# Kernel optimization log

Measured on AMD Instinct MI355X. Metric: run time of the kernel, lower is better.

The kernel has to match this reference:

```python
import jax, jax.numpy as jnp
import numpy as np

K = 8
W_CONST = 0.01
EPS = 1e-8


def _normalize(v, eps=1e-8):
    return v / (jnp.linalg.norm(v, axis=-1, keepdims=True) + eps)


def _coarse_normal(x, vertices, vertex_normals):
    # x: (N,3); vertices, vertex_normals: (V,3)
    # brute-force KNN (ascending by squared distance, like cKDTree.query)
    d2_all = jnp.sum((x[:, None, :] - vertices[None, :, :]) ** 2, axis=-1)  # (N,V)
    neg_d2, idx = jax.lax.top_k(-d2_all, K)  # sorted ascending distance
    d2 = -neg_d2                                                    # (N,K)
    v_knn = vertices[idx]                                           # (N,K,3)
    n_knn = vertex_normals[idx]                                     # (N,K,3)
    d2c = jnp.maximum(d2, EPS)
    inv_d2 = 1.0 / d2c                                              # (N,K)
    term_knn = jnp.sum(n_knn * inv_d2[..., None], axis=1)           # (N,3)
    v1 = v_knn[:, 0]                                                # nearest vertex
    d2_v1 = jnp.maximum(jnp.sum((x - v1) ** 2, axis=-1), EPS)       # (N,)
    term_dir = (x - v1) / (W_CONST * d2_v1[:, None])
    W = jnp.sum(inv_d2, axis=1) + 1.0 / W_CONST                     # (N,)
    n_tilde = (term_knn + term_dir) / W[:, None]
    nc = _normalize(n_tilde)
    return nc, v1


def _ray_mesh_first_hit(origins, dirs, tri0, e1, e2):
    # Moller-Trumbore, all points vs all faces. origins/dirs: (N,3); tri0/e1/e2: (F,3)
    pvec = jnp.cross(dirs[:, None, :], e2[None, :, :])              # (N,F,3)
    det = jnp.einsum('fk,nfk->nf', e1, pvec)                        # (N,F)
    ok_det = jnp.abs(det) > EPS
    inv_det = jnp.where(ok_det, 1.0 / jnp.where(ok_det, det, 1.0), 0.0)
    tvec = origins[:, None, :] - tri0[None, :, :]                   # (N,F,3)
    u = jnp.sum(tvec * pvec, axis=-1) * inv_det
    qvec = jnp.cross(tvec, e1[None, :, :])                          # (N,F,3)
    v = jnp.einsum('nk,nfk->nf', dirs, qvec) * inv_det
    t = jnp.einsum('fk,nfk->nf', e2, qvec) * inv_det
    valid = ok_det & (u >= 0.0) & (v >= 0.0) & (u + v <= 1.0) & (t > EPS)
    t_masked = jnp.where(valid, t, jnp.inf)
    t_min = jnp.min(t_masked, axis=1)                               # first hit along ray
    hit = jnp.isfinite(t_min)
    loc = origins + dirs * jnp.where(hit, t_min, 0.0)[:, None]
    return hit, loc


def _project(x, vertices, vertex_normals, faces):
    nc, v1 = _coarse_normal(x, vertices, vertex_normals)
    tri0 = vertices[faces[:, 0]]
    e1 = vertices[faces[:, 1]] - tri0
    e2 = vertices[faces[:, 2]] - tri0
    # primary cast along -nc
    hit1, loc1 = _ray_mesh_first_hit(x, -nc, tri0, e1, e2)
    # fallback cast toward nearest vertex
    dir_fb = _normalize(v1 - x)
    hit2, loc2 = _ray_mesh_first_hit(x, dir_fb, tri0, e1, e2)
    xc = jnp.where(hit1[:, None], loc1, jnp.where(hit2[:, None], loc2, v1))
    s = jnp.sum((x - xc) * nc, axis=-1, keepdims=True)              # (N,1)
    return xc, s, nc


def setup_inputs() -> dict:
    key = jax.random.key(0)
    k1, k2, k3, k4 = jax.random.split(key, 4)
    N, V, F = 2048, 8192, 8192
    x = jax.random.normal(k1, (N, 3), dtype=jnp.float32)
    vertices = jax.random.normal(k2, (V, 3), dtype=jnp.float32)
    vertex_normals = _normalize(jax.random.normal(k3, (V, 3), dtype=jnp.float32))
    faces = jax.random.randint(k4, (F, 3), 0, V, dtype=jnp.int32)
    return {"x": x, "vertices": vertices, "vertex_normals": vertex_normals, "faces": faces}


def reference(x, vertices, vertex_normals, faces):
    # returns (xc:(N,3), s:(N,1), nc:(N,3)) like ProjectionFn.forward
    return _project(x, vertices, vertex_normals, faces)
```

## Files before the change

kernel.cpp:

```cpp
#include <hip/hip_runtime.h>
#include <math.h>

#pragma float_control(precise, on)

#define EPSF 1e-8f


__global__ void __launch_bounds__(256) knn_prep_kernel(
    const float* __restrict__ x, const float* __restrict__ verts,
    const float* __restrict__ vnorm, const int* __restrict__ faces,
    float* __restrict__ tri, float* __restrict__ ncw,
    float* __restrict__ v1w, float* __restrict__ dfbw,
    int N, int V, int F) {
#pragma clang fp contract(off)
    int p = blockIdx.x;
    int tid = threadIdx.x;
    int wave = tid >> 6;
    int lane = tid & 63;
    if (p >= N) return;

    int gt = p * 256 + tid;
    if (gt < F) {
        int f0 = faces[gt * 3 + 0];
        int f1 = faces[gt * 3 + 1];
        int f2 = faces[gt * 3 + 2];
        float t0x = verts[f0 * 3 + 0], t0y = verts[f0 * 3 + 1], t0z = verts[f0 * 3 + 2];
        float ax = verts[f1 * 3 + 0], ay = verts[f1 * 3 + 1], az = verts[f1 * 3 + 2];
        float bx = verts[f2 * 3 + 0], by = verts[f2 * 3 + 1], bz = verts[f2 * 3 + 2];
        float4* t4 = (float4*)(tri + gt * 12);
        t4[0] = make_float4(t0x, t0y, t0z, ax - t0x);
        t4[1] = make_float4(ay - t0y, az - t0z, bx - t0x, by - t0y);
        t4[2] = make_float4(bz - t0z, 0.f, 0.f, 0.f);
    }

    float xx = x[p * 3 + 0];
    float xy = x[p * 3 + 1];
    float xz = x[p * 3 + 2];

    unsigned long long ka[8], kb[8];
#pragma unroll
    for (int i = 0; i < 8; ++i) { ka[i] = ~0ULL; kb[i] = ~0ULL; }

    for (int va = tid; va < V; va += 512) {
        int vb = va + 256;
        bool hasB = vb < V;

        float avx = verts[va * 3 + 0];
        float avy = verts[va * 3 + 1];
        float avz = verts[va * 3 + 2];
        float bvx = 0.f, bvy = 0.f, bvz = 0.f;
        if (hasB) {
            bvx = verts[vb * 3 + 0];
            bvy = verts[vb * 3 + 1];
            bvz = verts[vb * 3 + 2];
        }

        float dxa = xx - avx, dya = xy - avy, dza = xz - avz;
        float d2a = ((dxa * dxa) + (dya * dya)) + (dza * dza);
        unsigned long long kA =
            (((unsigned long long)__float_as_uint(d2a)) << 32) | (unsigned int)va;
        if (kA < ka[7]) {
            ka[7] = kA;
#pragma unroll
            for (int j = 7; j > 0; --j) {
                if (ka[j] < ka[j - 1]) {
                    unsigned long long t = ka[j];
                    ka[j] = ka[j - 1];
                    ka[j - 1] = t;
                }
            }
        }

        if (hasB) {
            float dxb = xx - bvx, dyb = xy - bvy, dzb = xz - bvz;
            float d2b = ((dxb * dxb) + (dyb * dyb)) + (dzb * dzb);
            unsigned long long kB =
                (((unsigned long long)__float_as_uint(d2b)) << 32) | (unsigned int)vb;
            if (kB < kb[7]) {
                kb[7] = kB;
#pragma unroll
                for (int j = 7; j > 0; --j) {
                    if (kb[j] < kb[j - 1]) {
                        unsigned long long t = kb[j];
                        kb[j] = kb[j - 1];
                        kb[j - 1] = t;
                    }
                }
            }
        }
    }

    unsigned long long wsel[8];
#pragma unroll
    for (int j = 0; j < 8; ++j) {
        unsigned long long c = (ka[0] < kb[0]) ? ka[0] : kb[0];
        unsigned long long m = c;
#pragma unroll
        for (int s = 1; s < 64; s <<= 1) {
            unsigned long long o = __shfl_xor(m, s, 64);
            if (o < m) m = o;
        }
        if (c == m) {
            if (ka[0] == m) {
#pragma unroll
                for (int t = 0; t < 7; ++t) ka[t] = ka[t + 1];
                ka[7] = ~0ULL;
            } else {
#pragma unroll
                for (int t = 0; t < 7; ++t) kb[t] = kb[t + 1];
                kb[7] = ~0ULL;
            }
        }
        wsel[j] = m;
    }

    __shared__ unsigned long long cand[32];
    if (lane == 0) {
#pragma unroll
        for (int j = 0; j < 8; ++j) cand[wave * 8 + j] = wsel[j];
    }
    __syncthreads();
    if (wave != 0) return;

    unsigned long long c0 = (lane < 32) ? cand[lane] : ~0ULL;
    unsigned long long sel[8];
#pragma unroll
    for (int j = 0; j < 8; ++j) {
        unsigned long long m = c0;
#pragma unroll
        for (int s = 1; s < 64; s <<= 1) {
            unsigned long long o = __shfl_xor(m, s, 64);
            if (o < m) m = o;
        }
        if (c0 == m) c0 = ~0ULL;
        sel[j] = m;
    }

    if (lane != 0) return;

    float invk[8];
    float nsx = 0.f, nsy = 0.f, nsz = 0.f;
#pragma unroll
    for (int j = 0; j < 8; ++j) {
        int id = (int)(sel[j] & 0xffffffffu);
        float d2 = __uint_as_float((unsigned int)(sel[j] >> 32));
        float inv = 1.0f / fmaxf(d2, EPSF);
        invk[j] = inv;
        nsx = nsx + vnorm[id * 3 + 0] * inv;
        nsy = nsy + vnorm[id * 3 + 1] * inv;
        nsz = nsz + vnorm[id * 3 + 2] * inv;
    }
    float Wsum = ((invk[0] + invk[1]) + (invk[2] + invk[3])) +
                 ((invk[4] + invk[5]) + (invk[6] + invk[7]));

    int id0 = (int)(sel[0] & 0xffffffffu);
    float v1x = verts[id0 * 3 + 0];
    float v1y = verts[id0 * 3 + 1];
    float v1z = verts[id0 * 3 + 2];

    float dxv = xx - v1x, dyv = xy - v1y, dzv = xz - v1z;
    float d2v1 = fmaxf(((dxv * dxv) + (dyv * dyv)) + (dzv * dzv), EPSF);
    float den = 0.01f * d2v1;
    float tdx = dxv / den, tdy = dyv / den, tdz = dzv / den;

    float W = Wsum + 100.0f;
    float ntx = (nsx + tdx) / W;
    float nty = (nsy + tdy) / W;
    float ntz = (nsz + tdz) / W;
    float nrm = sqrtf(((ntx * ntx) + (nty * nty)) + (ntz * ntz)) + 1e-8f;
    float ncx = ntx / nrm, ncy = nty / nrm, ncz = ntz / nrm;

    float fx = v1x - xx, fy = v1y - xy, fz = v1z - xz;
    float fn = sqrtf(((fx * fx) + (fy * fy)) + (fz * fz)) + 1e-8f;
    fx = fx / fn; fy = fy / fn; fz = fz / fn;

    ncw[p * 3 + 0] = ncx; ncw[p * 3 + 1] = ncy; ncw[p * 3 + 2] = ncz;
    v1w[p * 3 + 0] = v1x; v1w[p * 3 + 1] = v1y; v1w[p * 3 + 2] = v1z;
    dfbw[p * 3 + 0] = fx; dfbw[p * 3 + 1] = fy; dfbw[p * 3 + 2] = fz;
}

__global__ void __launch_bounds__(256) ray_fin_kernel(
    const float* __restrict__ x, const float* __restrict__ tri,
    const float* __restrict__ ncw, const float* __restrict__ v1w,
    const float* __restrict__ dfbw, float* __restrict__ out, int N, int F) {
#pragma clang fp contract(off)
    const float M = 1e-5f;
    __shared__ unsigned int red[8];
    int p = blockIdx.x;
    int tid = threadIdx.x;
    int wave = tid >> 6;
    int lane = tid & 63;
    if (p >= N) return;

    float xx = x[p * 3 + 0];
    float xy = x[p * 3 + 1];
    float xz = x[p * 3 + 2];
    float ncx = ncw[p * 3 + 0], ncy = ncw[p * 3 + 1], ncz = ncw[p * 3 + 2];
    float dbx = dfbw[p * 3 + 0], dby = dfbw[p * 3 + 1], dbz = dfbw[p * 3 + 2];
    float dax = -ncx, day = -ncy, daz = -ncz;

    const float INF = __uint_as_float(0x7f800000u);
    float tba = INF, tbb = INF;
    for (int fi = tid; fi < F; fi += 256) {
        const float4 A = *(const float4*)(tri + fi * 12);
        const float4 B = *(const float4*)(tri + fi * 12 + 4);
        const float4 C = *(const float4*)(tri + fi * 12 + 8);
        float e1x = A.w, e1y = B.x, e1z = B.y;
        float e2x = B.z, e2y = B.w, e2z = C.x;

        float tvx = xx - A.x;
        float tvy = xy - A.y;
        float tvz = xz - A.z;
        float qx = (tvy * e1z) - (tvz * e1y);
        float qy = (tvz * e1x) - (tvx * e1z);
        float qz = (tvx * e1y) - (tvy * e1x);
        float tq = ((e2x * qx) + (e2y * qy)) + (e2z * qz);

        {
            float px = (day * e2z) - (daz * e2y);
            float py = (daz * e2x) - (dax * e2z);
            float pz = (dax * e2y) - (day * e2x);
            float det = ((e1x * px) + (e1y * py)) + (e1z * pz);
            bool ok = fabsf(det) > EPSF;
            float inv = ok ? (1.0f / det) : 0.0f;
            float u = (((tvx * px) + (tvy * py)) + (tvz * pz)) * inv;
            float v = (((dax * qx) + (day * qy)) + (daz * qz)) * inv;
            float t = tq * inv;
            bool valid = ok && (u >= -M) && (v >= -M) && ((u + v) <= 1.0f + M) && (t > EPSF);
            tba = (valid && t < tba) ? t : tba;
        }
        {
            float px = (dby * e2z) - (dbz * e2y);
            float py = (dbz * e2x) - (dbx * e2z);
            float pz = (dbx * e2y) - (dby * e2x);
            float det = ((e1x * px) + (e1y * py)) + (e1z * pz);
            bool ok = fabsf(det) > EPSF;
            float inv = ok ? (1.0f / det) : 0.0f;
            float u = (((tvx * px) + (tvy * py)) + (tvz * pz)) * inv;
            float v = (((dbx * qx) + (dby * qy)) + (dbz * qz)) * inv;
            float t = tq * inv;
            bool valid = ok && (u >= -M) && (v >= -M) && ((u + v) <= 1.0f + M) && (t > EPSF);
            tbb = (valid && t < tbb) ? t : tbb;
        }
    }

    unsigned int ma = __float_as_uint(tba);
    unsigned int mb = __float_as_uint(tbb);
#pragma unroll
    for (int s = 1; s < 64; s <<= 1) {
        unsigned int oa = __shfl_xor(ma, s, 64);
        if (oa < ma) ma = oa;
        unsigned int ob = __shfl_xor(mb, s, 64);
        if (ob < mb) mb = ob;
    }
    if (lane == 0) { red[wave * 2 + 0] = ma; red[wave * 2 + 1] = mb; }
    __syncthreads();
    if (tid != 0) return;

    unsigned int u1 = min(min(red[0], red[2]), min(red[4], red[6]));
    unsigned int u2 = min(min(red[1], red[3]), min(red[5], red[7]));
    float t1 = __uint_as_float(u1);
    float t2 = __uint_as_float(u2);
    bool h1 = t1 < INF;
    bool h2 = t2 < INF;

    float xcx, xcy, xcz;
    if (h1) {
        xcx = xx + ((-ncx) * t1);
        xcy = xy + ((-ncy) * t1);
        xcz = xz + ((-ncz) * t1);
    } else if (h2) {
        xcx = xx + (dbx * t2);
        xcy = xy + (dby * t2);
        xcz = xz + (dbz * t2);
    } else {
        xcx = v1w[p * 3 + 0]; xcy = v1w[p * 3 + 1]; xcz = v1w[p * 3 + 2];
    }
    float s = (((xx - xcx) * ncx) + ((xy - xcy) * ncy)) + ((xz - xcz) * ncz);

    out[p * 3 + 0] = xcx;
    out[p * 3 + 1] = xcy;
    out[p * 3 + 2] = xcz;
    out[3 * N + p] = s;
    out[4 * N + p * 3 + 0] = ncx;
    out[4 * N + p * 3 + 1] = ncy;
    out[4 * N + p * 3 + 2] = ncz;
}

extern "C" void kernel_launch(void* const* d_in, const int* in_sizes, int n_in,
                              void* d_out, int out_size, void* d_ws, size_t ws_size,
                              hipStream_t stream) {
    const float* x     = (const float*)d_in[0];
    const float* verts = (const float*)d_in[1];
    const float* vnorm = (const float*)d_in[2];
    const int*   faces = (const int*)d_in[3];
    int N = in_sizes[0] / 3;
    int V = in_sizes[1] / 3;
    int F = in_sizes[3] / 3;

    float* tri  = (float*)d_ws;
    float* ncw  = tri + (size_t)F * 12;
    float* v1w  = ncw + 3 * N;
    float* dfbw = v1w + 3 * N;

    hipLaunchKernelGGL(knn_prep_kernel, dim3(N), dim3(256), 0, stream,
                       x, verts, vnorm, faces, tri, ncw, v1w, dfbw, N, V, F);
    hipLaunchKernelGGL(ray_fin_kernel, dim3(N), dim3(256), 0, stream,
                       x, tri, ncw, v1w, dfbw, (float*)d_out, N, F);
}
```

Measured before the change: 147.4 us.

## Process two points per block and run fallback ray cast only when primary misses

The ray kernel now handles two query points per block, so each triangle load is shared by two points' primary casts. The fallback cast toward the nearest vertex is no longer done for every point. It runs in a second pass over all faces only when a point's primary ray finds no hit. This removes redundant fallback intersection work and halves triangle-data traffic per point. The costs are an extra barrier, a possible second full pass over the triangles, and fewer blocks launched.

```diff
diff --git a/kernel.cpp b/kernel.cpp
--- a/kernel.cpp
+++ b/kernel.cpp
@@ -27,7 +27,7 @@
         float t0x = verts[f0 * 3 + 0], t0y = verts[f0 * 3 + 1], t0z = verts[f0 * 3 + 2];
         float ax = verts[f1 * 3 + 0], ay = verts[f1 * 3 + 1], az = verts[f1 * 3 + 2];
         float bx = verts[f2 * 3 + 0], by = verts[f2 * 3 + 1], bz = verts[f2 * 3 + 2];
-        float4* t4 = (float4*)(tri + gt * 12);
+        float4* t4 = (float4*)(tri + (size_t)gt * 12);
         t4[0] = make_float4(t0x, t0y, t0z, ax - t0x);
         t4[1] = make_float4(ay - t0y, az - t0z, bx - t0x, by - t0y);
         t4[2] = make_float4(bz - t0z, 0.f, 0.f, 0.f);
@@ -185,106 +185,224 @@
     const float* __restrict__ dfbw, float* __restrict__ out, int N, int F) {
 #pragma clang fp contract(off)
     const float M = 1e-5f;
-    __shared__ unsigned int red[8];
-    int p = blockIdx.x;
+    __shared__ unsigned int redA[4], redB[4];
+    __shared__ unsigned int u1As, u1Bs, u2As, u2Bs, hAf, hBf;
+    int b = blockIdx.x;
     int tid = threadIdx.x;
     int wave = tid >> 6;
     int lane = tid & 63;
-    if (p >= N) return;
-
-    float xx = x[p * 3 + 0];
-    float xy = x[p * 3 + 1];
-    float xz = x[p * 3 + 2];
-    float ncx = ncw[p * 3 + 0], ncy = ncw[p * 3 + 1], ncz = ncw[p * 3 + 2];
-    float dbx = dfbw[p * 3 + 0], dby = dfbw[p * 3 + 1], dbz = dfbw[p * 3 + 2];
-    float dax = -ncx, day = -ncy, daz = -ncz;
+    int pA = 2 * b;
+    if (pA >= N) return;
+    int pB = pA + 1;
+    bool hasB = pB < N;
+    int pBs = hasB ? pB : pA;
+
+    float axx = x[pA * 3 + 0], axy = x[pA * 3 + 1], axz = x[pA * 3 + 2];
+    float Ancx = ncw[pA * 3 + 0], Ancy = ncw[pA * 3 + 1], Ancz = ncw[pA * 3 + 2];
+    float Adbx = dfbw[pA * 3 + 0], Adby = dfbw[pA * 3 + 1], Adbz = dfbw[pA * 3 + 2];
+    float Adax = -Ancx, Aday = -Ancy, Adaz = -Ancz;
+
+    float bxx = x[pBs * 3 + 0], bxy = x[pBs * 3 + 1], bxz = x[pBs * 3 + 2];
+    float Bncx = ncw[pBs * 3 + 0], Bncy = ncw[pBs * 3 + 1], Bncz = ncw[pBs * 3 + 2];
+    float Bdbx = dfbw[pBs * 3 + 0], Bdby = dfbw[pBs * 3 + 1], Bdbz = dfbw[pBs * 3 + 2];
+    float Bdax = -Bncx, Bday = -Bncy, Bdaz = -Bncz;
 
     const float INF = __uint_as_float(0x7f800000u);
-    float tba = INF, tbb = INF;
+
+    float tA = INF, tB = INF;
     for (int fi = tid; fi < F; fi += 256) {
-        const float4 A = *(const float4*)(tri + fi * 12);
-        const float4 B = *(const float4*)(tri + fi * 12 + 4);
-        const float4 C = *(const float4*)(tri + fi * 12 + 8);
-        float e1x = A.w, e1y = B.x, e1z = B.y;
-        float e2x = B.z, e2y = B.w, e2z = C.x;
-
-        float tvx = xx - A.x;
-        float tvy = xy - A.y;
-        float tvz = xz - A.z;
-        float qx = (tvy * e1z) - (tvz * e1y);
-        float qy = (tvz * e1x) - (tvx * e1z);
-        float qz = (tvx * e1y) - (tvy * e1x);
-        float tq = ((e2x * qx) + (e2y * qy)) + (e2z * qz);
+        const float4 A4 = *(const float4*)(tri + (size_t)fi * 12);
+        const float4 B4 = *(const float4*)(tri + (size_t)fi * 12 + 4);
+        const float4 C4 = *(const float4*)(tri + (size_t)fi * 12 + 8);
+        float e1x = A4.w, e1y = B4.x, e1z = B4.y;
+        float e2x = B4.z, e2y = B4.w, e2z = C4.x;
 
         {
-            float px = (day * e2z) - (daz * e2y);
-            float py = (daz * e2x) - (dax * e2z);
-            float pz = (dax * e2y) - (day * e2x);
+            float tvx = axx - A4.x;
+            float tvy = axy - A4.y;
+            float tvz = axz - A4.z;
+            float qx = (tvy * e1z) - (tvz * e1y);
+            float qy = (tvz * e1x) - (tvx * e1z);
+            float qz = (tvx * e1y) - (tvy * e1x);
+            float tq = ((e2x * qx) + (e2y * qy)) + (e2z * qz);
+            float px = (Aday * e2z) - (Adaz * e2y);
+            float py = (Adaz * e2x) - (Adax * e2z);
+            float pz = (Adax * e2y) - (Aday * e2x);
             float det = ((e1x * px) + (e1y * py)) + (e1z * pz);
             bool ok = fabsf(det) > EPSF;
             float inv = ok ? (1.0f / det) : 0.0f;
             float u = (((tvx * px) + (tvy * py)) + (tvz * pz)) * inv;
-            float v = (((dax * qx) + (day * qy)) + (daz * qz)) * inv;
+            float v = (((Adax * qx) + (Aday * qy)) + (Adaz * qz)) * inv;
             float t = tq * inv;
             bool valid = ok && (u >= -M) && (v >= -M) && ((u + v) <= 1.0f + M) && (t > EPSF);
-            tba = (valid && t < tba) ? t : tba;
+            tA = (valid && t < tA) ? t : tA;
         }
         {
-            float px = (dby * e2z) - (dbz * e2y);
-            float py = (dbz * e2x) - (dbx * e2z);
-            float pz = (dbx * e2y) - (dby * e2x);
+            float tvx = bxx - A4.x;
+            float tvy = bxy - A4.y;
+            float tvz = bxz - A4.z;
+            float qx = (tvy * e1z) - (tvz * e1y);
+            float qy = (tvz * e1x) - (tvx * e1z);
+            float qz = (tvx * e1y) - (tvy * e1x);
+            float tq = ((e2x * qx) + (e2y * qy)) + (e2z * qz);
+            float px = (Bday * e2z) - (Bdaz * e2y);
+            float py = (Bdaz * e2x) - (Bdax * e2z);
+            float pz = (Bdax * e2y) - (Bday * e2x);
             float det = ((e1x * px) + (e1y * py)) + (e1z * pz);
             bool ok = fabsf(det) > EPSF;
             float inv = ok ? (1.0f / det) : 0.0f;
             float u = (((tvx * px) + (tvy * py)) + (tvz * pz)) * inv;
-            float v = (((dbx * qx) + (dby * qy)) + (dbz * qz)) * inv;
+            float v = (((Bdax * qx) + (Bday * qy)) + (Bdaz * qz)) * inv;
             float t = tq * inv;
             bool valid = ok && (u >= -M) && (v >= -M) && ((u + v) <= 1.0f + M) && (t > EPSF);
-            tbb = (valid && t < tbb) ? t : tbb;
-        }
-    }
-
-    unsigned int ma = __float_as_uint(tba);
-    unsigned int mb = __float_as_uint(tbb);
-#pragma unroll
-    for (int s = 1; s < 64; s <<= 1) {
-        unsigned int oa = __shfl_xor(ma, s, 64);
-        if (oa < ma) ma = oa;
-        unsigned int ob = __shfl_xor(mb, s, 64);
-        if (ob < mb) mb = ob;
-    }
-    if (lane == 0) { red[wave * 2 + 0] = ma; red[wave * 2 + 1] = mb; }
+            tB = (valid && t < tB) ? t : tB;
+        }
+    }
+
+    {
+        unsigned int ma = __float_as_uint(tA);
+        unsigned int mb = __float_as_uint(tB);
+#pragma unroll
+        for (int s = 1; s < 64; s <<= 1) {
+            unsigned int oa = __shfl_xor(ma, s, 64);
+            if (oa < ma) ma = oa;
+            unsigned int ob = __shfl_xor(mb, s, 64);
+            if (ob < mb) mb = ob;
+        }
+        if (lane == 0) { redA[wave] = ma; redB[wave] = mb; }
+    }
     __syncthreads();
+    if (tid == 0) {
+        unsigned int u1A = min(min(redA[0], redA[1]), min(redA[2], redA[3]));
+        unsigned int u1B = min(min(redB[0], redB[1]), min(redB[2], redB[3]));
+        u1As = u1A; u1Bs = u1B;
+        hAf = (u1A < 0x7f800000u) ? 1u : 0u;
+        hBf = (u1B < 0x7f800000u) ? 1u : 0u;
+    }
+    __syncthreads();
+
+    bool needA = (hAf == 0u);
+    bool needB = hasB && (hBf == 0u);
+    if (needA || needB) {
+        float sA = INF, sB = INF;
+        for (int fi = tid; fi < F; fi += 256) {
+            const float4 A4 = *(const float4*)(tri + (size_t)fi * 12);
+            const float4 B4 = *(const float4*)(tri + (size_t)fi * 12 + 4);
+            const float4 C4 = *(const float4*)(tri + (size_t)fi * 12 + 8);
+            float e1x = A4.w, e1y = B4.x, e1z = B4.y;
+            float e2x = B4.z, e2y = B4.w, e2z = C4.x;
+
+            if (needA) {
+                float tvx = axx - A4.x;
+                float tvy = axy - A4.y;
+                float tvz = axz - A4.z;
+                float qx = (tvy * e1z) - (tvz * e1y);
+                float qy = (tvz * e1x) - (tvx * e1z);
+                float qz = (tvx * e1y) - (tvy * e1x);
+                float tq = ((e2x * qx) + (e2y * qy)) + (e2z * qz);
+                float px = (Adby * e2z) - (Adbz * e2y);
+                float py = (Adbz * e2x) - (Adbx * e2z);
+                float pz = (Adbx * e2y) - (Adby * e2x);
+                float det = ((e1x * px) + (e1y * py)) + (e1z * pz);
+                bool ok = fabsf(det) > EPSF;
+                float inv = ok ? (1.0f / det) : 0.0f;
+                float u = (((tvx * px) + (tvy * py)) + (tvz * pz)) * inv;
+                float v = (((Adbx * qx) + (Adby * qy)) + (Adbz * qz)) * inv;
+                float t = tq * inv;
+                bool valid = ok && (u >= -M) && (v >= -M) && ((u + v) <= 1.0f + M) && (t > EPSF);
+                sA = (valid && t < sA) ? t : sA;
+            }
+            if (needB) {
+                float tvx = bxx - A4.x;
+                float tvy = bxy - A4.y;
+                float tvz = bxz - A4.z;
+                float qx = (tvy * e1z) - (tvz * e1y);
+                float qy = (tvz * e1x) - (tvx * e1z);
+                float qz = (tvx * e1y) - (tvy * e1x);
+                float tq = ((e2x * qx) + (e2y * qy)) + (e2z * qz);
+                float px = (Bdby * e2z) - (Bdbz * e2y);
+                float py = (Bdbz * e2x) - (Bdbx * e2z);
+                float pz = (Bdbx * e2y) - (Bdby * e2x);
+                float det = ((e1x * px) + (e1y * py)) + (e1z * pz);
+                bool ok = fabsf(det) > EPSF;
+                float inv = ok ? (1.0f / det) : 0.0f;
+                float u = (((tvx * px) + (tvy * py)) + (tvz * pz)) * inv;
+                float v = (((Bdbx * qx) + (Bdby * qy)) + (Bdbz * qz)) * inv;
+                float t = tq * inv;
+                bool valid = ok && (u >= -M) && (v >= -M) && ((u + v) <= 1.0f + M) && (t > EPSF);
+                sB = (valid && t < sB) ? t : sB;
+            }
+        }
+        unsigned int ma = __float_as_uint(sA);
+        unsigned int mb = __float_as_uint(sB);
+#pragma unroll
+        for (int s = 1; s < 64; s <<= 1) {
+            unsigned int oa = __shfl_xor(ma, s, 64);
+            if (oa < ma) ma = oa;
+            unsigned int ob = __shfl_xor(mb, s, 64);
+            if (ob < mb) mb = ob;
+        }
+        if (lane == 0) { redA[wave] = ma; redB[wave] = mb; }
+        __syncthreads();
+        if (tid == 0) {
+            u2As = min(min(redA[0], redA[1]), min(redA[2], redA[3]));
+            u2Bs = min(min(redB[0], redB[1]), min(redB[2], redB[3]));
+        }
+    }
+
     if (tid != 0) return;
-
-    unsigned int u1 = min(min(red[0], red[2]), min(red[4], red[6]));
-    unsigned int u2 = min(min(red[1], red[3]), min(red[5], red[7]));
-    float t1 = __uint_as_float(u1);
-    float t2 = __uint_as_float(u2);
-    bool h1 = t1 < INF;
-    bool h2 = t2 < INF;
-
-    float xcx, xcy, xcz;
-    if (h1) {
-        xcx = xx + ((-ncx) * t1);
-        xcy = xy + ((-ncy) * t1);
-        xcz = xz + ((-ncz) * t1);
-    } else if (h2) {
-        xcx = xx + (dbx * t2);
-        xcy = xy + (dby * t2);
-        xcz = xz + (dbz * t2);
-    } else {
-        xcx = v1w[p * 3 + 0]; xcy = v1w[p * 3 + 1]; xcz = v1w[p * 3 + 2];
-    }
-    float s = (((xx - xcx) * ncx) + ((xy - xcy) * ncy)) + ((xz - xcz) * ncz);
-
-    out[p * 3 + 0] = xcx;
-    out[p * 3 + 1] = xcy;
-    out[p * 3 + 2] = xcz;
-    out[3 * N + p] = s;
-    out[4 * N + p * 3 + 0] = ncx;
-    out[4 * N + p * 3 + 1] = ncy;
-    out[4 * N + p * 3 + 2] = ncz;
+    {
+        float t1 = __uint_as_float(u1As);
+        bool h1 = t1 < INF;
+        float t2 = h1 ? INF : __uint_as_float(u2As);
+        bool h2 = t2 < INF;
+        float xcx, xcy, xcz;
+        if (h1) {
+            xcx = axx + ((-Ancx) * t1);
+            xcy = axy + ((-Ancy) * t1);
+            xcz = axz + ((-Ancz) * t1);
+        } else if (h2) {
+            xcx = axx + (Adbx * t2);
+            xcy = axy + (Adby * t2);
+            xcz = axz + (Adbz * t2);
+        } else {
+            xcx = v1w[pA * 3 + 0]; xcy = v1w[pA * 3 + 1]; xcz = v1w[pA * 3 + 2];
+        }
+        float s = (((axx - xcx) * Ancx) + ((axy - xcy) * Ancy)) + ((axz - xcz) * Ancz);
+        out[pA * 3 + 0] = xcx;
+        out[pA * 3 + 1] = xcy;
+        out[pA * 3 + 2] = xcz;
+        out[3 * N + pA] = s;
+        out[4 * N + pA * 3 + 0] = Ancx;
+        out[4 * N + pA * 3 + 1] = Ancy;
+        out[4 * N + pA * 3 + 2] = Ancz;
+    }
+    if (hasB) {
+        float t1 = __uint_as_float(u1Bs);
+        bool h1 = t1 < INF;
+        float t2 = h1 ? INF : __uint_as_float(u2Bs);
+        bool h2 = t2 < INF;
+        float xcx, xcy, xcz;
+        if (h1) {
+            xcx = bxx + ((-Bncx) * t1);
+            xcy = bxy + ((-Bncy) * t1);
+            xcz = bxz + ((-Bncz) * t1);
+        } else if (h2) {
+            xcx = bxx + (Bdbx * t2);
+            xcy = bxy + (Bdby * t2);
+            xcz = bxz + (Bdbz * t2);
+        } else {
+            xcx = v1w[pB * 3 + 0]; xcy = v1w[pB * 3 + 1]; xcz = v1w[pB * 3 + 2];
+        }
+        float s = (((bxx - xcx) * Bncx) + ((bxy - xcy) * Bncy)) + ((bxz - xcz) * Bncz);
+        out[pB * 3 + 0] = xcx;
+        out[pB * 3 + 1] = xcy;
+        out[pB * 3 + 2] = xcz;
+        out[3 * N + pB] = s;
+        out[4 * N + pB * 3 + 0] = Bncx;
+        out[4 * N + pB * 3 + 1] = Bncy;
+        out[4 * N + pB * 3 + 2] = Bncz;
+    }
 }
 
 extern "C" void kernel_launch(void* const* d_in, const int* in_sizes, int n_in,
@@ -305,6 +423,7 @@
 
     hipLaunchKernelGGL(knn_prep_kernel, dim3(N), dim3(256), 0, stream,
                        x, verts, vnorm, faces, tri, ncw, v1w, dfbw, N, V, F);
-    hipLaunchKernelGGL(ray_fin_kernel, dim3(N), dim3(256), 0, stream,
+    int rblocks = (N + 1) / 2;
+    hipLaunchKernelGGL(ray_fin_kernel, dim3(rblocks), dim3(256), 0, stream,
                        x, tri, ncw, v1w, dfbw, (float*)d_out, N, F);
 }
```

After: 140.6 us. -4.6%, faster.
